# Performance work log

Hardware: AMD Instinct MI355X
Metric: run time of the kernel (lower is better)

## Reference

```python
import jax, jax.numpy as jnp
import numpy as np

H = 4        # num_heads
DH = 64      # output_dim (d_head)
D = 256      # input_dim (hidden)
NUM_LAYERS = 2


def _gru_cell(x, h, Wih, Whh, bih, bhh):
    # PyTorch GRUCell: gates ordered (r, z, n)
    gi = x @ Wih.T + bih
    gh = h @ Whh.T + bhh
    i_r, i_z, i_n = jnp.split(gi, 3, axis=-1)
    h_r, h_z, h_n = jnp.split(gh, 3, axis=-1)
    r = jax.nn.sigmoid(i_r + h_r)
    z = jax.nn.sigmoid(i_z + h_z)
    n = jnp.tanh(i_n + r * h_n)
    return (1.0 - z) * n + z * h


def _mha(x, attn_mask, Wq, bq, Wk, bk, Wv, bv, Wo):
    B, N, _ = x.shape
    q = (x @ Wq.T + bq).reshape(B, N, H, DH)
    k = (x @ Wk.T + bk).reshape(B, N, H, DH)
    v = (x @ Wv.T + bv).reshape(B, N, H, DH)
    # scores computed in fp32 (autocast disabled in original)
    scores = jnp.einsum('bnhd,bmhd->bhnm', q.astype(jnp.float32), k.astype(jnp.float32)) / jnp.float32(DH) ** 0.5
    scores = jnp.where(attn_mask[:, None], jnp.float32(-1e9), scores)  # mask broadcast over heads
    attn = jax.nn.softmax(scores, axis=-1)
    ctx = jnp.einsum('bhnm,bmhd->bnhd', attn, v).reshape(B, N, H * DH)
    return ctx @ Wo.T  # W_O has no bias


def setup_inputs() -> dict:
    B, N = 1024, 128
    key = jax.random.key(0)
    ks = jax.random.split(key, 14)
    s = 0.02
    return {
        'latent': jax.random.normal(ks[0], (B, N, D), jnp.float32),
        'comm_mask': jax.random.randint(ks[1], (B, N, N), 0, 2) > 0,
        'trait_weight': jax.random.normal(ks[2], (B, N), jnp.float32),
        'Wq': jax.random.normal(ks[3], (H * DH, D), jnp.float32) * s,
        'bq': jnp.zeros((H * DH,), jnp.float32),
        'Wk': jax.random.normal(ks[4], (H * DH, D), jnp.float32) * s,
        'bk': jnp.zeros((H * DH,), jnp.float32),
        'Wv': jax.random.normal(ks[5], (H * DH, D), jnp.float32) * s,
        'bv': jnp.zeros((H * DH,), jnp.float32),
        'Wo': jax.random.normal(ks[6], (DH, H * DH), jnp.float32) * s,
        'Wih': jax.random.normal(ks[7], (3 * D, DH), jnp.float32) * s,
        'Whh': jax.random.normal(ks[8], (3 * D, D), jnp.float32) * s,
        'bih': jnp.zeros((3 * D,), jnp.float32),
        'bhh': jnp.zeros((3 * D,), jnp.float32),
    }


def reference(latent, comm_mask, trait_weight, Wq, bq, Wk, bk, Wv, bv, Wo, Wih, Whh, bih, bhh):
    B, N, _ = latent.shape
    attn_mask = ~comm_mask                                    # [B,N,N] True = blocked
    update_mask = (comm_mask.sum(axis=-1) > 1)[..., None]     # [B,N,1]
    for _ in range(NUM_LAYERS):
        info = _mha(latent, attn_mask, Wq, bq, Wk, bk, Wv, bv, Wo)          # [B,N,DH]
        upd = _gru_cell(info.reshape(-1, DH), latent.reshape(-1, D), Wih, Whh, bih, bhh)
        latent = jnp.where(update_mask, upd.reshape(B, N, D), latent)
    return latent
```

## Files before the change

### kernel.cpp

```cpp
#include <hip/hip_runtime.h>
#include <stdint.h>

#define NTOK 128
#define DHID 256
#define NHEAD 4
#define DHEAD 64

typedef short bf16x8 __attribute__((ext_vector_type(8)));
typedef float f32x4 __attribute__((ext_vector_type(4)));

#define MFMA(a,b,c) __builtin_amdgcn_mfma_f32_16x16x32_bf16((a),(b),(c),0,0,0)

__device__ __forceinline__ float bf2f(uint16_t u){
  union { uint32_t i; float f; } v; v.i = ((uint32_t)u) << 16; return v.f;
}
__device__ __forceinline__ uint16_t f2bf(float f){
  union { uint32_t i; float f; } v; v.f = f;
  uint32_t i = v.i + 0x7FFFu + ((v.i >> 16) & 1u);
  return (uint16_t)(i >> 16);
}

__global__ void k_detect(const uint32_t* __restrict__ raw, uint32_t* __restrict__ flag){
  int lane = threadIdx.x;
  int hits = 0;
  #pragma unroll
  for (int i = 0; i < 16; i++){
    uint32_t w = raw[lane*16 + i];
    uint32_t e = (w >> 7) & 0xFFu;
    hits += (e >= 0x70u && e <= 0x8Fu) ? 1 : 0;
  }
  #pragma unroll
  for (int m = 1; m < 64; m <<= 1) hits += __shfl_xor(hits, m);
  if (lane == 0) *flag = (hits > 512) ? 1u : 0u;
}

__global__ void k_conv(const void* __restrict__ src, unsigned long long off,
                       uint16_t* __restrict__ dst, const uint32_t* __restrict__ flag, int n){
  const int isbf = (int)*flag;
  int i0 = (blockIdx.x * blockDim.x + threadIdx.x) * 8;
  int stride = gridDim.x * blockDim.x * 8;
  if (isbf){
    const uint16_t* s = (const uint16_t*)src + off;
    for (int i = i0; i < n; i += stride)
      *(bf16x8*)(dst + i) = *(const bf16x8*)(s + i);
  } else {
    const float* s = (const float*)src + off;
    for (int i = i0; i < n; i += stride){
      float4 a = *(const float4*)(s + i);
      float4 b = *(const float4*)(s + i + 4);
      uint16_t o[8] = {f2bf(a.x),f2bf(a.y),f2bf(a.z),f2bf(a.w),
                       f2bf(b.x),f2bf(b.y),f2bf(b.z),f2bf(b.w)};
      *(bf16x8*)(dst + i) = *(const bf16x8*)o;
    }
  }
}

__global__ void k_store(const uint16_t* __restrict__ L, void* __restrict__ dst,
                        unsigned long long off, const uint32_t* __restrict__ flag, int n){
  const int isbf = (int)*flag;
  int i0 = (blockIdx.x * blockDim.x + threadIdx.x) * 8;
  int stride = gridDim.x * blockDim.x * 8;
  if (isbf){
    uint16_t* d = (uint16_t*)dst + off;
    for (int i = i0; i < n; i += stride)
      *(bf16x8*)(d + i) = *(const bf16x8*)(L + i);
  } else {
    float* d = (float*)dst + off;
    for (int i = i0; i < n; i += stride){
      bf16x8 v = *(const bf16x8*)(L + i);
      #pragma unroll
      for (int e = 0; e < 8; e++) d[i + e] = bf2f((uint16_t)v[e]);
    }
  }
}

__global__ __launch_bounds__(256) void k_maskpack(const int* __restrict__ mask,
                                                  unsigned long long* __restrict__ packed,
                                                  unsigned char* __restrict__ upd, int nrows){
  int row = blockIdx.x * 4 + (threadIdx.x >> 6);
  if (row >= nrows) return;
  int lane = threadIdx.x & 63;
  const int* mrow = mask + (size_t)row * NTOK;
  unsigned long long b0 = __ballot(mrow[lane] != 0);
  unsigned long long b1 = __ballot(mrow[lane + 64] != 0);
  if (lane == 0){
    packed[row*2 + 0] = b0;
    packed[row*2 + 1] = b1;
    upd[row] = (unsigned char)((__popcll(b0) + __popcll(b1)) > 1 ? 1 : 0);
  }
}

__global__ __launch_bounds__(256) void k_qkv(
    const uint16_t* __restrict__ X,
    const uint16_t* __restrict__ Wq, const uint16_t* __restrict__ bq,
    const uint16_t* __restrict__ Wk, const uint16_t* __restrict__ bk,
    const uint16_t* __restrict__ Wv, const uint16_t* __restrict__ bv,
    uint16_t* __restrict__ Oq, uint16_t* __restrict__ Ok, uint16_t* __restrict__ Ov)
{
  extern __shared__ uint16_t sm[];
  uint16_t* Xs = sm;
  uint16_t* Ws = sm + 64*256;
  const int r0 = blockIdx.x * 64;
  const int tid = threadIdx.x;
  const int lane = tid & 63, lr = lane & 15, lg = lane >> 4;
  const int wav = tid >> 6;
  const int wr = (wav >> 1) * 32, wc = (wav & 1) * 32;

  #pragma unroll
  for (int i = 0; i < 8; i++){
    int c = tid + i*256, row = c >> 5, g = c & 31;
    *(bf16x8*)(Xs + row*256 + (g ^ (row & 7))*8) =
        *(const bf16x8*)(X + (size_t)(r0+row)*DHID + g*8);
  }

  bf16x8 wreg[8];
  auto wptr = [&](int t)->const uint16_t*{
    int w = t >> 2;
    return (w == 0) ? Wq : ((w == 1) ? Wk : Wv);
  };
  auto preload = [&](int t){
    const uint16_t* W = wptr(t);
    int c0t = (t & 3) * 64;
    #pragma unroll
    for (int i = 0; i < 8; i++){
      int idx = tid + i*256, r = idx >> 5, g = idx & 31;
      wreg[i] = *(const bf16x8*)(W + (size_t)(c0t + r)*DHID + g*8);
    }
  };
  preload(0);

  for (int t = 0; t < 12; t++){
    __syncthreads();
    #pragma unroll
    for (int i = 0; i < 8; i++){
      int idx = tid + i*256, r = idx >> 5, g = idx & 31;
      *(bf16x8*)(Ws + r*256 + ((g ^ (r & 7))*8)) = wreg[i];
    }
    __syncthreads();
    if (t < 11) preload(t+1);

    f32x4 acc[2][2] = {};
    #pragma unroll
    for (int kk = 0; kk < 8; kk++){
      int off = ((kk*4 + lg) ^ (lr & 7)) * 8;
      bf16x8 a0 = *(const bf16x8*)(Xs + (wr +      lr)*256 + off);
      bf16x8 a1 = *(const bf16x8*)(Xs + (wr + 16 + lr)*256 + off);
      bf16x8 b0 = *(const bf16x8*)(Ws + (wc +      lr)*256 + off);
      bf16x8 b1 = *(const bf16x8*)(Ws + (wc + 16 + lr)*256 + off);
      acc[0][0] = MFMA(a0, b0, acc[0][0]);
      acc[0][1] = MFMA(a0, b1, acc[0][1]);
      acc[1][0] = MFMA(a1, b0, acc[1][0]);
      acc[1][1] = MFMA(a1, b1, acc[1][1]);
    }
    int w = t >> 2, c0t = (t & 3) * 64;
    const uint16_t* bias = (w == 0) ? bq : ((w == 1) ? bk : bv);
    uint16_t* O = (w == 0) ? Oq : ((w == 1) ? Ok : Ov);
    #pragma unroll
    for (int i = 0; i < 2; i++)
    #pragma unroll
    for (int j = 0; j < 2; j++){
      int col = c0t + wc + j*16 + lr;
      float bvv = bf2f(bias[col]);
      #pragma unroll
      for (int rr = 0; rr < 4; rr++){
        int row = r0 + wr + i*16 + lg*4 + rr;
        O[(size_t)row*DHID + col] = f2bf(acc[i][j][rr] + bvv);
      }
    }
  }
}

__global__ __launch_bounds__(256) void k_attn(
    const uint16_t* __restrict__ Q, const uint16_t* __restrict__ Kb, const uint16_t* __restrict__ V,
    const unsigned long long* __restrict__ packed, uint16_t* __restrict__ ctx)
{
  extern __shared__ uint16_t sm[];
  uint16_t* Ks = sm;
  uint16_t* Vt = sm + 128*64;
  uint16_t* Ps = Vt + 64*128;
  const int b = blockIdx.x >> 2;
  const int h = blockIdx.x & 3;
  const int tid = threadIdx.x, lane = tid & 63, wav = tid >> 6;
  const int lr = lane & 15, lg = lane >> 4;
  const size_t base = ((size_t)b * NTOK) * DHID + h * DHEAD;

  #pragma unroll
  for (int i = 0; i < 4; i++){
    int c = tid + i*256;
    int row = c >> 3, g = c & 7;
    *(bf16x8*)(Ks + row*64 + (g ^ (row & 7))*8) =
        *(const bf16x8*)(Kb + base + (size_t)row*DHID + g*8);
  }
  #pragma unroll
  for (int i = 0; i < 4; i++){
    int c = tid + i*256;
    int n = c & 127, d8 = (c >> 7) * 8;
    bf16x8 v = *(const bf16x8*)(V + base + (size_t)n*DHID + d8);
    #pragma unroll
    for (int e = 0; e < 8; e++){
      int d = d8 + e;
      Vt[d*128 + ((n >> 3) ^ (d & 7))*8 + (n & 7)] = (uint16_t)v[e];
    }
  }
  __syncthreads();

  const int qrow0 = wav * 32;
  bf16x8 qf[2][2];
  #pragma unroll
  for (int i = 0; i < 2; i++)
  #pragma unroll
  for (int kk = 0; kk < 2; kk++)
    qf[i][kk] = *(const bf16x8*)(Q + base + (size_t)(qrow0 + i*16 + lr)*DHID + kk*32 + lg*8);

  f32x4 sa[2][8] = {};
  #pragma unroll
  for (int kk = 0; kk < 2; kk++){
    int off = ((kk*4 + lg) ^ (lr & 7)) * 8;
    #pragma unroll
    for (int j = 0; j < 8; j++){
      bf16x8 bf = *(const bf16x8*)(Ks + (j*16 + lr)*64 + off);
      sa[0][j] = MFMA(qf[0][kk], bf, sa[0][j]);
      sa[1][j] = MFMA(qf[1][kk], bf, sa[1][j]);
    }
  }
  #pragma unroll
  for (int i = 0; i < 2; i++){
    #pragma unroll
    for (int rr = 0; rr < 4; rr++){
      int n = qrow0 + i*16 + lg*4 + rr;
      unsigned long long m0 = packed[((size_t)b*NTOK + n)*2 + 0];
      unsigned long long m1 = packed[((size_t)b*NTOK + n)*2 + 1];
      float sv[8];
      float mx = -3.0e38f;
      #pragma unroll
      for (int j = 0; j < 8; j++){
        int col = j*16 + lr;
        unsigned long long w = (col < 64) ? m0 : m1;
        float s = sa[i][j][rr] * 0.125f;
        sv[j] = ((w >> (col & 63)) & 1ull) ? s : -1e9f;
        mx = fmaxf(mx, sv[j]);
      }
      mx = fmaxf(mx, __shfl_xor(mx, 1));
      mx = fmaxf(mx, __shfl_xor(mx, 2));
      mx = fmaxf(mx, __shfl_xor(mx, 4));
      mx = fmaxf(mx, __shfl_xor(mx, 8));
      float sum = 0.f;
      #pragma unroll
      for (int j = 0; j < 8; j++){ sv[j] = __expf(sv[j] - mx); sum += sv[j]; }
      sum += __shfl_xor(sum, 1);
      sum += __shfl_xor(sum, 2);
      sum += __shfl_xor(sum, 4);
      sum += __shfl_xor(sum, 8);
      float inv = __builtin_amdgcn_rcpf(sum);
      #pragma unroll
      for (int j = 0; j < 8; j++){
        int col = j*16 + lr;
        Ps[n*128 + ((col >> 3) ^ (n & 7))*8 + (col & 7)] = f2bf(sv[j] * inv);
      }
    }
  }
  __syncthreads();

  f32x4 oa[2][4] = {};
  #pragma unroll
  for (int kk = 0; kk < 4; kk++){
    int off = ((kk*4 + lg) ^ (lr & 7)) * 8;
    bf16x8 a0 = *(const bf16x8*)(Ps + (qrow0 +      lr)*128 + off);
    bf16x8 a1 = *(const bf16x8*)(Ps + (qrow0 + 16 + lr)*128 + off);
    #pragma unroll
    for (int j = 0; j < 4; j++){
      bf16x8 bf = *(const bf16x8*)(Vt + (j*16 + lr)*128 + off);
      oa[0][j] = MFMA(a0, bf, oa[0][j]);
      oa[1][j] = MFMA(a1, bf, oa[1][j]);
    }
  }
  #pragma unroll
  for (int i = 0; i < 2; i++)
  #pragma unroll
  for (int j = 0; j < 4; j++)
  #pragma unroll
  for (int rr = 0; rr < 4; rr++){
    int n = qrow0 + i*16 + lg*4 + rr;
    ctx[((size_t)b*NTOK + n)*DHID + h*DHEAD + j*16 + lr] = f2bf(oa[i][j][rr]);
  }
}

__global__ __launch_bounds__(512, 4) void k_gru(
    const uint16_t* __restrict__ ctxp, const uint16_t* __restrict__ lat,
    const uint16_t* __restrict__ Wo, const uint16_t* __restrict__ Wih, const uint16_t* __restrict__ Whh,
    const uint16_t* __restrict__ bih, const uint16_t* __restrict__ bhh,
    const unsigned char* __restrict__ upd, uint16_t* __restrict__ lat_out)
{
  extern __shared__ uint16_t sm[];
  uint16_t* WhhS  = sm;
  uint16_t* WihS  = sm + 12288;
  uint16_t* Is    = sm + 15360;
  uint16_t* biasS = sm + 23552;
  const int r0 = blockIdx.x * 128;
  const int tid = threadIdx.x, lane = tid & 63, wav = tid >> 6;
  const int lr = lane & 15, lg = lane >> 4;
  const int wrow = wav * 16;

  #pragma unroll
  for (int i = 0; i < 3; i++){
    int idx = tid + i*512;
    if (idx < 1536) biasS[idx] = (idx < 768) ? bih[idx] : bhh[idx - 768];
  }

  bf16x8 wreg[4];
  auto preload = [&](int cs){
    #pragma unroll
    for (int i = 0; i < 4; i++){
      int idx = tid + i*512;
      if (idx < 1536){
        int r = idx >> 5, gc = idx & 31;
        wreg[i] = *(const bf16x8*)(Whh + (size_t)((r>>4)*256 + cs*16 + (r&15))*DHID + gc*8);
      } else if (idx < 1920){
        int j2 = idx - 1536, r = j2 >> 3, gc = j2 & 7;
        wreg[i] = *(const bf16x8*)(Wih + (size_t)((r>>4)*256 + cs*16 + (r&15))*DHEAD + gc*8);
      }
    }
  };
  auto stagew = [&](){
    #pragma unroll
    for (int i = 0; i < 4; i++){
      int idx = tid + i*512;
      if (idx < 1536){
        int r = idx >> 5, gc = idx & 31;
        *(bf16x8*)(WhhS + r*256 + ((gc ^ (r&7))*8)) = wreg[i];
      } else if (idx < 1920){
        int j2 = idx - 1536, r = j2 >> 3, gc = j2 & 7;
        *(bf16x8*)(WihS + r*64 + ((gc ^ (r&7))*8)) = wreg[i];
      }
    }
  };
  preload(0);

  bf16x8 aL[8], actx[8];
  #pragma unroll
  for (int kk = 0; kk < 8; kk++){
    size_t rowb = (size_t)(r0 + wrow + lr);
    aL[kk]   = *(const bf16x8*)(lat  + rowb*DHID + kk*32 + lg*8);
    actx[kk] = *(const bf16x8*)(ctxp + rowb*DHID + kk*32 + lg*8);
  }
  uint32_t u4;
  {
    const unsigned char* up = upd + r0 + wrow + lg*4;
    u4 = (uint32_t)up[0] | ((uint32_t)up[1]<<8) | ((uint32_t)up[2]<<16) | ((uint32_t)up[3]<<24);
  }

  f32x4 ai[4] = {};
  #pragma unroll
  for (int kk = 0; kk < 8; kk++){
    #pragma unroll
    for (int j = 0; j < 4; j++){
      bf16x8 b = *(const bf16x8*)(Wo + (size_t)(j*16 + lr)*DHID + kk*32 + lg*8);
      ai[j] = MFMA(actx[kk], b, ai[j]);
    }
  }
  #pragma unroll
  for (int j = 0; j < 4; j++)
  #pragma unroll
  for (int rr = 0; rr < 4; rr++){
    int row = wrow + lg*4 + rr, col = j*16 + lr;
    Is[row*64 + ((col>>3) ^ (row&7))*8 + (col&7)] = f2bf(ai[j][rr]);
  }
  stagew();
  __syncthreads();

  bf16x8 aI[2];
  #pragma unroll
  for (int kk = 0; kk < 2; kk++)
    aI[kk] = *(const bf16x8*)(Is + (wrow + lr)*64 + ((kk*4 + lg) ^ (lr&7))*8);

  const float LOG2E = 1.44269504f;
  for (int cs = 0; cs < 16; cs++){
    if (cs < 15) preload(cs+1);
    f32x4 gi[3] = {}, gh[3] = {};
    #pragma unroll
    for (int kk = 0; kk < 2; kk++)
    #pragma unroll
    for (int g = 0; g < 3; g++){
      bf16x8 b = *(const bf16x8*)(WihS + (g*16+lr)*64 + ((kk*4+lg)^(lr&7))*8);
      gi[g] = MFMA(aI[kk], b, gi[g]);
    }
    #pragma unroll
    for (int kk = 0; kk < 8; kk++)
    #pragma unroll
    for (int g = 0; g < 3; g++){
      bf16x8 b = *(const bf16x8*)(WhhS + (g*16+lr)*256 + ((kk*4+lg)^(lr&7))*8);
      gh[g] = MFMA(aL[kk], b, gh[g]);
    }
    int col = cs*16 + lr;
    float bir = bf2f(biasS[col]),     biz = bf2f(biasS[256+col]),  bin_ = bf2f(biasS[512+col]);
    float bhr = bf2f(biasS[768+col]), bhz = bf2f(biasS[1024+col]), bhn  = bf2f(biasS[1280+col]);
    #pragma unroll
    for (int rr = 0; rr < 4; rr++){
      int row = wrow + lg*4 + rr;
      float hv = bf2f(lat[(size_t)(r0+row)*DHID + col]);
      float xr = (gi[0][rr]+bir) + (gh[0][rr]+bhr);
      float xz = (gi[1][rr]+biz) + (gh[1][rr]+bhz);
      float rg = __builtin_amdgcn_rcpf(1.f + __builtin_amdgcn_exp2f(-xr*LOG2E));
      float zg = __builtin_amdgcn_rcpf(1.f + __builtin_amdgcn_exp2f(-xz*LOG2E));
      float nx = (gi[2][rr]+bin_) + rg*(gh[2][rr]+bhn);
      nx = fminf(10.f, fmaxf(-10.f, nx));
      float e2 = __builtin_amdgcn_exp2f(-2.f*LOG2E*nx);
      float ng = (1.f - e2) * __builtin_amdgcn_rcpf(1.f + e2);
      float hp = (1.f - zg)*ng + zg*hv;
      float ov = ((u4 >> (rr*8)) & 1u) ? hp : hv;
      lat_out[(size_t)(r0+row)*DHID + col] = f2bf(ov);
    }
    __syncthreads();
    if (cs < 15){ stagew(); __syncthreads(); }
  }
}

extern "C" void kernel_launch(void* const* d_in, const int* in_sizes, int n_in,
                              void* d_out, int out_size, void* d_ws, size_t ws_size,
                              hipStream_t stream)
{
  (void)in_sizes; (void)n_in; (void)out_size;
  const void* latent = d_in[0];
  const int*  mask   = (const int*)d_in[1];
  const void* Wq  = d_in[3]; const void* bq  = d_in[4];
  const void* Wk  = d_in[5]; const void* bk  = d_in[6];
  const void* Wv  = d_in[7]; const void* bv  = d_in[8];
  const void* Wo  = d_in[9];
  const void* Wih = d_in[10]; const void* Whh = d_in[11];
  const void* bih = d_in[12]; const void* bhh = d_in[13];

  uint8_t* p = (uint8_t*)d_ws;
  uint32_t* flag = (uint32_t*)p;            p += 256;
  uint16_t* Wqc  = (uint16_t*)p;            p += 65536*2;
  uint16_t* Wkc  = (uint16_t*)p;            p += 65536*2;
  uint16_t* Wvc  = (uint16_t*)p;            p += 65536*2;
  uint16_t* Woc  = (uint16_t*)p;            p += 16384*2;
  uint16_t* Wihc = (uint16_t*)p;            p += 49152*2;
  uint16_t* Whhc = (uint16_t*)p;            p += 196608*2;
  uint16_t* bqc  = (uint16_t*)p;            p += 512;
  uint16_t* bkc  = (uint16_t*)p;            p += 512;
  uint16_t* bvc  = (uint16_t*)p;            p += 512;
  uint16_t* bihc = (uint16_t*)p;            p += 1536;
  uint16_t* bhhc = (uint16_t*)p;            p += 1536;
  uint8_t* chunk0 = p;
  size_t reserved = (size_t)(chunk0 - (uint8_t*)d_ws);
  const size_t perb = 5ull*65536 + 2048 + 128;

  const int Btot = 1024;
  int CB = (int)((ws_size > reserved ? ws_size - reserved : 0) / perb);
  if (CB > Btot) CB = Btot;
  if (CB < 1)    CB = 1;

  auto cgrid = [](int n){ int b = (n/8 + 255)/256; if (b > 2048) b = 2048; if (b < 1) b = 1; return (unsigned)b; };

  k_detect<<<1, 64, 0, stream>>>((const uint32_t*)latent, flag);
  k_conv<<<cgrid(65536), 256, 0, stream>>>(Wq, 0, Wqc, flag, 65536);
  k_conv<<<cgrid(65536), 256, 0, stream>>>(Wk, 0, Wkc, flag, 65536);
  k_conv<<<cgrid(65536), 256, 0, stream>>>(Wv, 0, Wvc, flag, 65536);
  k_conv<<<cgrid(16384), 256, 0, stream>>>(Wo, 0, Woc, flag, 16384);
  k_conv<<<cgrid(49152), 256, 0, stream>>>(Wih, 0, Wihc, flag, 49152);
  k_conv<<<cgrid(196608),256, 0, stream>>>(Whh, 0, Whhc, flag, 196608);
  k_conv<<<1, 256, 0, stream>>>(bq, 0, bqc, flag, 256);
  k_conv<<<1, 256, 0, stream>>>(bk, 0, bkc, flag, 256);
  k_conv<<<1, 256, 0, stream>>>(bv, 0, bvc, flag, 256);
  k_conv<<<1, 256, 0, stream>>>(bih, 0, bihc, flag, 768);
  k_conv<<<1, 256, 0, stream>>>(bhh, 0, bhhc, flag, 768);

  for (int b0 = 0; b0 < Btot; b0 += CB){
    int cb = (Btot - b0 < CB) ? (Btot - b0) : CB;
    int rows = cb * 128;
    int nelem = rows * DHID;
    uint8_t* q = chunk0;
    uint16_t* L    = (uint16_t*)q; q += (size_t)cb*65536;
    uint16_t* q_ws = (uint16_t*)q; q += (size_t)cb*65536;
    uint16_t* k_ws = (uint16_t*)q; q += (size_t)cb*65536;
    uint16_t* v_ws = (uint16_t*)q; q += (size_t)cb*65536;
    uint16_t* c_ws = (uint16_t*)q; q += (size_t)cb*65536;
    unsigned long long* packed = (unsigned long long*)q; q += (size_t)cb*2048;
    unsigned char* updp = (unsigned char*)q;

    k_conv<<<cgrid(nelem), 256, 0, stream>>>(latent, (unsigned long long)b0*NTOK*DHID, L, flag, nelem);
    k_maskpack<<<dim3(rows/4), 256, 0, stream>>>(mask + (size_t)b0*NTOK*NTOK, packed, updp, rows);

    for (int layer = 0; layer < 2; layer++){
      k_qkv <<<dim3(rows/64),  256, 65536, stream>>>(L, Wqc,bqc, Wkc,bkc, Wvc,bvc, q_ws, k_ws, v_ws);
      k_attn<<<dim3(cb*NHEAD), 256, 65536, stream>>>(q_ws, k_ws, v_ws, packed, c_ws);
      k_gru <<<dim3(rows/128), 512, 50176, stream>>>(c_ws, L, Woc, Wihc, Whhc, bihc, bhhc, updp, L);
    }
    k_store<<<cgrid(nelem), 256, 0, stream>>>(L, d_out, (unsigned long long)b0*NTOK*DHID, flag, nelem);
  }
}
```

Measured before the change: 766.3 us.

## Enlarge GRU row tile and double-buffer weights via async global-to-LDS loads

Each GRU block now handles 512 rows instead of 128, with each wave covering four 16-row tiles. Every staged weight chunk is therefore reused across four times as many rows, which cuts global weight traffic. Weight chunks are double-buffered in LDS and filled with direct global_load_lds transfers, removing the register round-trip and one barrier per chunk step. The r and z gate input and hidden products now share one accumulator. In exchange the kernel uses about 131 KB of LDS and many more VGPRs, launches a quarter as many blocks, and requires the batch chunk size to be a multiple of four.

```diff
diff --git a/kernel.cpp b/kernel.cpp
--- a/kernel.cpp
+++ b/kernel.cpp
@@ -285,21 +285,21 @@
   }
 }
 
-__global__ __launch_bounds__(512, 4) void k_gru(
+__global__ __launch_bounds__(512, 2) void k_gru(
     const uint16_t* __restrict__ ctxp, const uint16_t* __restrict__ lat,
     const uint16_t* __restrict__ Wo, const uint16_t* __restrict__ Wih, const uint16_t* __restrict__ Whh,
     const uint16_t* __restrict__ bih, const uint16_t* __restrict__ bhh,
     const unsigned char* __restrict__ upd, uint16_t* __restrict__ lat_out)
 {
   extern __shared__ uint16_t sm[];
-  uint16_t* WhhS  = sm;
-  uint16_t* WihS  = sm + 12288;
-  uint16_t* Is    = sm + 15360;
-  uint16_t* biasS = sm + 23552;
-  const int r0 = blockIdx.x * 128;
+  uint16_t* Wb0   = sm;
+  uint16_t* Wb1   = sm + 16384;
+  uint16_t* Is    = sm + 32768;
+  uint16_t* biasS = sm + 65536;
+  const int r0 = blockIdx.x * 512;
   const int tid = threadIdx.x, lane = tid & 63, wav = tid >> 6;
   const int lr = lane & 15, lg = lane >> 4;
-  const int wrow = wav * 16;
+  const int wrow = wav * 64;
 
   #pragma unroll
   for (int i = 0; i < 3; i++){
@@ -307,111 +307,129 @@
     if (idx < 1536) biasS[idx] = (idx < 768) ? bih[idx] : bhh[idx - 768];
   }
 
-  bf16x8 wreg[4];
-  auto preload = [&](int cs){
-    #pragma unroll
-    for (int i = 0; i < 4; i++){
-      int idx = tid + i*512;
-      if (idx < 1536){
-        int r = idx >> 5, gc = idx & 31;
-        wreg[i] = *(const bf16x8*)(Whh + (size_t)((r>>4)*256 + cs*16 + (r&15))*DHID + gc*8);
-      } else if (idx < 1920){
-        int j2 = idx - 1536, r = j2 >> 3, gc = j2 & 7;
-        wreg[i] = *(const bf16x8*)(Wih + (size_t)((r>>4)*256 + cs*16 + (r&15))*DHEAD + gc*8);
+  auto stage_async = [&](int cs, uint16_t* buf){
+    #pragma unroll
+    for (int c = 0; c < 4; c++){
+      int G = wav*256 + c*64 + lane;
+      const uint16_t* src;
+      if (G < 1536){
+        int r = G >> 5, gp = G & 31;
+        src = Whh + (size_t)((r>>4)*256 + cs*16 + (r&15))*DHID + (gp ^ (r&7))*8;
+      } else if (G < 1920){
+        int G2 = G - 1536, r = G2 >> 3, gp = G2 & 7;
+        src = Wih + (size_t)((r>>4)*256 + cs*16 + (r&15))*DHEAD + (gp ^ (r&7))*8;
+      } else {
+        src = Whh;
       }
+      __builtin_amdgcn_global_load_lds(
+          (const __attribute__((address_space(1))) uint32_t*)src,
+          (__attribute__((address_space(3))) uint32_t*)(buf + (size_t)(wav*256 + c*64)*8),
+          16, 0, 0);
     }
   };
-  auto stagew = [&](){
-    #pragma unroll
-    for (int i = 0; i < 4; i++){
-      int idx = tid + i*512;
-      if (idx < 1536){
-        int r = idx >> 5, gc = idx & 31;
-        *(bf16x8*)(WhhS + r*256 + ((gc ^ (r&7))*8)) = wreg[i];
-      } else if (idx < 1920){
-        int j2 = idx - 1536, r = j2 >> 3, gc = j2 & 7;
-        *(bf16x8*)(WihS + r*64 + ((gc ^ (r&7))*8)) = wreg[i];
-      }
-    }
-  };
-  preload(0);
-
-  bf16x8 aL[8], actx[8];
+
+  f32x4 ai[4][4] = {};
   #pragma unroll
   for (int kk = 0; kk < 8; kk++){
-    size_t rowb = (size_t)(r0 + wrow + lr);
-    aL[kk]   = *(const bf16x8*)(lat  + rowb*DHID + kk*32 + lg*8);
-    actx[kk] = *(const bf16x8*)(ctxp + rowb*DHID + kk*32 + lg*8);
-  }
-  uint32_t u4;
-  {
-    const unsigned char* up = upd + r0 + wrow + lg*4;
-    u4 = (uint32_t)up[0] | ((uint32_t)up[1]<<8) | ((uint32_t)up[2]<<16) | ((uint32_t)up[3]<<24);
-  }
-
-  f32x4 ai[4] = {};
-  #pragma unroll
-  for (int kk = 0; kk < 8; kk++){
-    #pragma unroll
-    for (int j = 0; j < 4; j++){
-      bf16x8 b = *(const bf16x8*)(Wo + (size_t)(j*16 + lr)*DHID + kk*32 + lg*8);
-      ai[j] = MFMA(actx[kk], b, ai[j]);
-    }
-  }
+    bf16x8 bw[4];
+    #pragma unroll
+    for (int j = 0; j < 4; j++)
+      bw[j] = *(const bf16x8*)(Wo + (size_t)(j*16 + lr)*DHID + kk*32 + lg*8);
+    #pragma unroll
+    for (int t = 0; t < 4; t++){
+      bf16x8 ac = *(const bf16x8*)(ctxp + (size_t)(r0 + wrow + t*16 + lr)*DHID + kk*32 + lg*8);
+      #pragma unroll
+      for (int j = 0; j < 4; j++) ai[t][j] = MFMA(ac, bw[j], ai[t][j]);
+    }
+  }
+  #pragma unroll
+  for (int t = 0; t < 4; t++)
   #pragma unroll
   for (int j = 0; j < 4; j++)
   #pragma unroll
   for (int rr = 0; rr < 4; rr++){
-    int row = wrow + lg*4 + rr, col = j*16 + lr;
-    Is[row*64 + ((col>>3) ^ (row&7))*8 + (col&7)] = f2bf(ai[j][rr]);
-  }
-  stagew();
+    int row = wrow + t*16 + lg*4 + rr, col = j*16 + lr;
+    Is[row*64 + ((col>>3) ^ (row&7))*8 + (col&7)] = f2bf(ai[t][j][rr]);
+  }
+
+  bf16x8 aL[4][8];
+  #pragma unroll
+  for (int t = 0; t < 4; t++)
+  #pragma unroll
+  for (int kk = 0; kk < 8; kk++)
+    aL[t][kk] = *(const bf16x8*)(lat + (size_t)(r0 + wrow + t*16 + lr)*DHID + kk*32 + lg*8);
+
+  uint32_t u4[4];
+  #pragma unroll
+  for (int t = 0; t < 4; t++)
+    u4[t] = *(const uint32_t*)(upd + r0 + wrow + t*16 + lg*4);
+
+  stage_async(0, Wb0);
   __syncthreads();
-
-  bf16x8 aI[2];
-  #pragma unroll
-  for (int kk = 0; kk < 2; kk++)
-    aI[kk] = *(const bf16x8*)(Is + (wrow + lr)*64 + ((kk*4 + lg) ^ (lr&7))*8);
 
   const float LOG2E = 1.44269504f;
   for (int cs = 0; cs < 16; cs++){
-    if (cs < 15) preload(cs+1);
-    f32x4 gi[3] = {}, gh[3] = {};
-    #pragma unroll
-    for (int kk = 0; kk < 2; kk++)
-    #pragma unroll
-    for (int g = 0; g < 3; g++){
-      bf16x8 b = *(const bf16x8*)(WihS + (g*16+lr)*64 + ((kk*4+lg)^(lr&7))*8);
-      gi[g] = MFMA(aI[kk], b, gi[g]);
-    }
-    #pragma unroll
-    for (int kk = 0; kk < 8; kk++)
-    #pragma unroll
-    for (int g = 0; g < 3; g++){
-      bf16x8 b = *(const bf16x8*)(WhhS + (g*16+lr)*256 + ((kk*4+lg)^(lr&7))*8);
-      gh[g] = MFMA(aL[kk], b, gh[g]);
-    }
+    uint16_t* Wcur = (cs & 1) ? Wb1 : Wb0;
+    if (cs < 15) stage_async(cs+1, (cs & 1) ? Wb0 : Wb1);
+
+    const uint16_t* WhhS = Wcur;
+    const uint16_t* WihS = Wcur + 12288;
+
+    f32x4 arz[2][4] = {};
+    f32x4 gin[4] = {}, ghn[4] = {};
+
+    #pragma unroll
+    for (int kk = 0; kk < 2; kk++){
+      int off = ((kk*4 + lg) ^ (lr & 7)) * 8;
+      bf16x8 br = *(const bf16x8*)(WihS + (0*16 + lr)*64 + off);
+      bf16x8 bz = *(const bf16x8*)(WihS + (1*16 + lr)*64 + off);
+      bf16x8 bn = *(const bf16x8*)(WihS + (2*16 + lr)*64 + off);
+      #pragma unroll
+      for (int t = 0; t < 4; t++){
+        bf16x8 a = *(const bf16x8*)(Is + (wrow + t*16 + lr)*64 + off);
+        arz[0][t] = MFMA(a, br, arz[0][t]);
+        arz[1][t] = MFMA(a, bz, arz[1][t]);
+        gin[t]    = MFMA(a, bn, gin[t]);
+      }
+    }
+    #pragma unroll
+    for (int kk = 0; kk < 8; kk++){
+      int off = ((kk*4 + lg) ^ (lr & 7)) * 8;
+      bf16x8 br = *(const bf16x8*)(WhhS + (0*16 + lr)*256 + off);
+      bf16x8 bz = *(const bf16x8*)(WhhS + (1*16 + lr)*256 + off);
+      bf16x8 bn = *(const bf16x8*)(WhhS + (2*16 + lr)*256 + off);
+      #pragma unroll
+      for (int t = 0; t < 4; t++){
+        arz[0][t] = MFMA(aL[t][kk], br, arz[0][t]);
+        arz[1][t] = MFMA(aL[t][kk], bz, arz[1][t]);
+        ghn[t]    = MFMA(aL[t][kk], bn, ghn[t]);
+      }
+    }
+
     int col = cs*16 + lr;
-    float bir = bf2f(biasS[col]),     biz = bf2f(biasS[256+col]),  bin_ = bf2f(biasS[512+col]);
-    float bhr = bf2f(biasS[768+col]), bhz = bf2f(biasS[1024+col]), bhn  = bf2f(biasS[1280+col]);
+    float brz0 = bf2f(biasS[col])     + bf2f(biasS[768+col]);
+    float brz1 = bf2f(biasS[256+col]) + bf2f(biasS[1024+col]);
+    float bin_ = bf2f(biasS[512+col]);
+    float bhn  = bf2f(biasS[1280+col]);
+    #pragma unroll
+    for (int t = 0; t < 4; t++)
     #pragma unroll
     for (int rr = 0; rr < 4; rr++){
-      int row = wrow + lg*4 + rr;
+      int row = wrow + t*16 + lg*4 + rr;
       float hv = bf2f(lat[(size_t)(r0+row)*DHID + col]);
-      float xr = (gi[0][rr]+bir) + (gh[0][rr]+bhr);
-      float xz = (gi[1][rr]+biz) + (gh[1][rr]+bhz);
+      float xr = arz[0][t][rr] + brz0;
+      float xz = arz[1][t][rr] + brz1;
       float rg = __builtin_amdgcn_rcpf(1.f + __builtin_amdgcn_exp2f(-xr*LOG2E));
       float zg = __builtin_amdgcn_rcpf(1.f + __builtin_amdgcn_exp2f(-xz*LOG2E));
-      float nx = (gi[2][rr]+bin_) + rg*(gh[2][rr]+bhn);
+      float nx = (gin[t][rr] + bin_) + rg*(ghn[t][rr] + bhn);
       nx = fminf(10.f, fmaxf(-10.f, nx));
       float e2 = __builtin_amdgcn_exp2f(-2.f*LOG2E*nx);
       float ng = (1.f - e2) * __builtin_amdgcn_rcpf(1.f + e2);
       float hp = (1.f - zg)*ng + zg*hv;
-      float ov = ((u4 >> (rr*8)) & 1u) ? hp : hv;
+      float ov = ((u4[t] >> (rr*8)) & 1u) ? hp : hv;
       lat_out[(size_t)(r0+row)*DHID + col] = f2bf(ov);
     }
     __syncthreads();
-    if (cs < 15){ stagew(); __syncthreads(); }
   }
 }
 
@@ -449,7 +467,8 @@
   const int Btot = 1024;
   int CB = (int)((ws_size > reserved ? ws_size - reserved : 0) / perb);
   if (CB > Btot) CB = Btot;
-  if (CB < 1)    CB = 1;
+  CB &= ~3;
+  if (CB < 4) CB = 4;
 
   auto cgrid = [](int n){ int b = (n/8 + 255)/256; if (b > 2048) b = 2048; if (b < 1) b = 1; return (unsigned)b; };
 
@@ -483,9 +502,9 @@
     k_maskpack<<<dim3(rows/4), 256, 0, stream>>>(mask + (size_t)b0*NTOK*NTOK, packed, updp, rows);
 
     for (int layer = 0; layer < 2; layer++){
-      k_qkv <<<dim3(rows/64),  256, 65536, stream>>>(L, Wqc,bqc, Wkc,bkc, Wvc,bvc, q_ws, k_ws, v_ws);
-      k_attn<<<dim3(cb*NHEAD), 256, 65536, stream>>>(q_ws, k_ws, v_ws, packed, c_ws);
-      k_gru <<<dim3(rows/128), 512, 50176, stream>>>(c_ws, L, Woc, Wihc, Whhc, bihc, bhhc, updp, L);
+      k_qkv <<<dim3(rows/64),  256, 65536,  stream>>>(L, Wqc,bqc, Wkc,bkc, Wvc,bvc, q_ws, k_ws, v_ws);
+      k_attn<<<dim3(cb*NHEAD), 256, 65536,  stream>>>(q_ws, k_ws, v_ws, packed, c_ws);
+      k_gru <<<dim3(rows/512), 512, 134144, stream>>>(c_ws, L, Woc, Wihc, Whhc, bihc, bhhc, updp, L);
     }
     k_store<<<cgrid(nelem), 256, 0, stream>>>(L, d_out, (unsigned long long)b0*NTOK*DHID, flag, nelem);
   }
```

Result: slower. 850.9 us (+11.0%).
